# Performance work log

Hardware: AMD Instinct MI355X
Metric: run time of the kernel (lower is better)

Reference implementation:

```python
import math
import jax, jax.numpy as jnp
import numpy as np

SCALE = math.sqrt(128.0)  # NOTE: original code MULTIPLIES by sqrt(128)
DROPOUT_P = 0.1


def setup_inputs() -> dict:
    key = jax.random.key(0)
    kq, kk, kv = jax.random.split(key, 3)
    B, Q, V, H = 4, 4096, 4096, 128
    return {
        "query": jax.random.normal(kq, (B, Q, H), dtype=jnp.float32),
        "key": jax.random.normal(kk, (B, V, H), dtype=jnp.float32),
        "value": jax.random.normal(kv, (B, V, H), dtype=jnp.float32),
    }


def reference(query, key, value):
    # qk: [B, Q, V]
    qk = jnp.einsum("bqh,bvh->bqv", query, key)
    scaled_qk = qk * SCALE
    softmax_qk = jax.nn.softmax(scaled_qk, axis=-1)
    # inverted dropout with a fixed RNG key (deterministic reference)
    dk = jax.random.key(42)
    keep = jax.random.bernoulli(dk, 1.0 - DROPOUT_P, softmax_qk.shape)
    dropout_qk = jnp.where(keep, softmax_qk / (1.0 - DROPOUT_P), 0.0)
    # output: [B, Q, H]
    return jnp.einsum("bqv,bvh->bqh", dropout_qk, value)
```

## Files before the change

kernel.cpp:

```cpp
#include <hip/hip_runtime.h>
#include <stdint.h>

#define NBATCH 4
#define NQ 4096
#define NV 4096
#define HD 128

#define SCL2E ((float)(11.31370849898476 * 1.4426950408889634))

#define KEEP_THRESH 3865470464u
#define EPS_SKIP 1e-6f

#define CHK_K(v,c) ((((v) * 16) + (((c) ^ (v)) & 15)) * 8)
#define CHK_V(h,c) ((((h) * 8)  + (((c) ^ (h)) & 7))  * 8)
#define TILE_USH 24576
#define WS_NEEDED ((size_t)NBATCH * 64 * TILE_USH * 2)

#define PSTR2 40
#define VLSTR 142

#define KSTR 144
#define VSTR 76
#define PSTR 72

typedef __attribute__((ext_vector_type(8))) short short8;
typedef __attribute__((ext_vector_type(4))) float floatx4;
typedef unsigned int uint;
typedef unsigned short ushort;
typedef __attribute__((address_space(3))) uint lds_u32;
typedef __attribute__((address_space(1))) const uint glb_u32;

__device__ __forceinline__ ushort bf16rne(float f) {
    uint u = __float_as_uint(f);
    u = (u + 0x7fffu + ((u >> 16) & 1u)) >> 16;
    return (ushort)u;
}
__device__ __forceinline__ float bf2f(ushort h) {
    return __uint_as_float(((uint)h) << 16);
}

template <int CTRL>
__device__ __forceinline__ float dppmov(float x) {
    return __int_as_float(__builtin_amdgcn_update_dpp(
        0, __float_as_int(x), CTRL, 0xF, 0xF, true));
}
__device__ __forceinline__ float row_max16(float x) {
    x = fmaxf(x, dppmov<0xB1>(x));
    x = fmaxf(x, dppmov<0x4E>(x));
    x = fmaxf(x, dppmov<0x141>(x));
    x = fmaxf(x, dppmov<0x140>(x));
    return x;
}
__device__ __forceinline__ float row_sum16(float x) {
    x += dppmov<0xB1>(x);
    x += dppmov<0x4E>(x);
    x += dppmov<0x141>(x);
    x += dppmov<0x140>(x);
    return x;
}

__device__ __forceinline__ uint rotl(uint x, int r) { return (x << r) | (x >> (32 - r)); }

__device__ __forceinline__ uint threefry_bits(uint j) {
    uint x0 = 0u;
    uint x1 = j;
    const uint k0 = 0u, k1 = 42u, k2 = 0u ^ 42u ^ 0x1BD11BDAu;
    x0 += k0; x1 += k1;
#define TFR4(a,b,c,d) \
    x0 += x1; x1 = rotl(x1, a); x1 ^= x0; \
    x0 += x1; x1 = rotl(x1, b); x1 ^= x0; \
    x0 += x1; x1 = rotl(x1, c); x1 ^= x0; \
    x0 += x1; x1 = rotl(x1, d); x1 ^= x0;
    TFR4(13, 15, 26, 6)
    x0 += k1; x1 += k2 + 1u;
    TFR4(17, 29, 16, 24)
    x0 += k2; x1 += k0 + 2u;
    TFR4(13, 15, 26, 6)
    x0 += k0; x1 += k1 + 3u;
    TFR4(17, 29, 16, 24)
    x0 += k1; x1 += k2 + 4u;
    TFR4(13, 15, 26, 6)
    x0 += k2; x1 += k0 + 5u;
#undef TFR4
    return x0 ^ x1;
}

__global__ __launch_bounds__(256)
void prepass(const float* __restrict__ Kg, const float* __restrict__ Vg,
             ushort* __restrict__ W) {
    __shared__ ushort vls[64 * VLSTR];
    const int rec  = blockIdx.x >> 1;
    const int half = blockIdx.x & 1;
    const int bb = rec >> 6;
    const int t  = rec & 63;
    const int v0 = t * 64;
    const size_t kvbase = (size_t)bb * NV * HD;
    ushort* dst = W + ((size_t)bb * 64 + t) * TILE_USH;
    const int tid = threadIdx.x;

    if (half == 0) {
        ushort* dkh = dst;
        ushort* dkl = dst + 8192;
#pragma unroll
        for (int i = 0; i < 4; ++i) {
            int lc = i * 256 + tid;
            int v = lc >> 4, c = lc & 15;
            const float* src = Kg + kvbase + (size_t)(v0 + v) * HD + c * 8;
            float x[8];
            *(float4*)&x[0] = *(const float4*)src;
            *(float4*)&x[4] = *(const float4*)(src + 4);
            uint H[4], L[4];
#pragma unroll
            for (int k = 0; k < 4; ++k) {
                ushort h0 = bf16rne(x[2 * k]),     h1 = bf16rne(x[2 * k + 1]);
                ushort l0 = bf16rne(x[2 * k] - bf2f(h0));
                ushort l1 = bf16rne(x[2 * k + 1] - bf2f(h1));
                H[k] = (uint)h0 | ((uint)h1 << 16);
                L[k] = (uint)l0 | ((uint)l1 << 16);
            }
            int pos = CHK_K(v, c);
            *(uint4*)&dkh[pos] = *(uint4*)H;
            *(uint4*)&dkl[pos] = *(uint4*)L;
        }
    } else {
        ushort* dvt = dst + 16384;
#pragma unroll
        for (int i = 0; i < 8; ++i) {
            int idx = i * 256 + tid;
            int v = idx >> 5, hq = idx & 31;
            float4 a = *(const float4*)(Vg + kvbase + (size_t)(v0 + v) * HD + hq * 4);
            uint w0 = (uint)bf16rne(a.x) | ((uint)bf16rne(a.y) << 16);
            uint w1 = (uint)bf16rne(a.z) | ((uint)bf16rne(a.w) << 16);
            *(uint*)&vls[v * VLSTR + hq * 4]     = w0;
            *(uint*)&vls[v * VLSTR + hq * 4 + 2] = w1;
        }
        __syncthreads();
#pragma unroll
        for (int i = 0; i < 4; ++i) {
            int oc = i * 256 + tid;
            int h = oc >> 3, swz = oc & 7;
            int c2 = (swz ^ h) & 7;
            uint Wd[4];
#pragma unroll
            for (int m = 0; m < 8; m += 2) {
                ushort a  = vls[(c2 * 8 + m) * VLSTR + h];
                ushort b2 = vls[(c2 * 8 + m + 1) * VLSTR + h];
                Wd[m >> 1] = (uint)a | ((uint)b2 << 16);
            }
            *(uint4*)&dvt[oc * 8] = *(uint4*)Wd;
        }
    }
}

__global__ __launch_bounds__(256, 2)
void fa_mfma5(const float* __restrict__ Qg, const ushort* __restrict__ Wk,
              float* __restrict__ Og) {
    __shared__ __align__(16) ushort kbuf[16384];
    __shared__ __align__(16) ushort vbuf[2][8192];
    __shared__ ushort pls[4][16 * PSTR2];
    __shared__ float mrow[4][32];

    const int tid  = threadIdx.x;
    const int wave = tid >> 6;
    const int lane = tid & 63;
    const int r    = lane & 15;
    const int qd   = lane >> 4;
    const int rg   = wave >> 1;
    const int cw   = wave & 1;
    const int blockRow0 = blockIdx.x * 32;
    const int b = blockRow0 >> 12;
    const int waveRow0 = blockRow0 + rg * 16;
    const ushort* kvw = Wk + (size_t)b * 64 * TILE_USH;

    short8 qfh[4], qfl[4];
    {
        const float* qp = Qg + (size_t)(waveRow0 + r) * HD + qd * 8;
#pragma unroll
        for (int kc = 0; kc < 4; ++kc) {
            float x[8];
            *(float4*)&x[0] = *(const float4*)(qp + kc * 32);
            *(float4*)&x[4] = *(const float4*)(qp + kc * 32 + 4);
#pragma unroll
            for (int j = 0; j < 8; ++j) {
                ushort h = bf16rne(x[j]);
                qfh[kc][j] = (short)h;
                qfl[kc][j] = (short)bf16rne(x[j] - bf2f(h));
            }
        }
    }

    floatx4 oacc[8];
#pragma unroll
    for (int n = 0; n < 8; ++n) oacc[n] = (floatx4){0.f, 0.f, 0.f, 0.f};
    float m2[4] = {-INFINITY, -INFINITY, -INFINITY, -INFINITY};
    float lr[4] = {0.f, 0.f, 0.f, 0.f};

#define STAGE(tt, vs) do { \
        const ushort* _sK = kvw + (size_t)(tt) * TILE_USH; \
        const ushort* _sV = _sK + 16384; \
        _Pragma("unroll") \
        for (int _i = 0; _i < 8; ++_i) \
            __builtin_amdgcn_global_load_lds((glb_u32*)(_sK + (_i * 256 + tid) * 8), \
                (lds_u32*)&kbuf[(_i * 256 + wave * 64) * 8], 16, 0, 0); \
        _Pragma("unroll") \
        for (int _i = 0; _i < 4; ++_i) \
            __builtin_amdgcn_global_load_lds((glb_u32*)(_sV + (_i * 256 + tid) * 8), \
                (lds_u32*)&vbuf[vs][(_i * 256 + wave * 64) * 8], 16, 0, 0); \
    } while (0)

    STAGE(0, 0);

    for (int t = 0; t < 64; ++t) {
        __syncthreads();

        const ushort* KH = kbuf;
        const ushort* KL = kbuf + 8192;
        const int v0 = t * 64;

        floatx4 cf[2];
        cf[0] = (floatx4){0.f, 0.f, 0.f, 0.f};
        cf[1] = (floatx4){0.f, 0.f, 0.f, 0.f};
#pragma unroll
        for (int kc = 0; kc < 4; ++kc) {
#pragma unroll
            for (int nb = 0; nb < 2; ++nb) {
                int ch = CHK_K(cw * 32 + nb * 16 + r, kc * 4 + qd);
                short8 kh = *(const short8*)&KH[ch];
                short8 kl = *(const short8*)&KL[ch];
                cf[nb] = __builtin_amdgcn_mfma_f32_16x16x32_bf16(qfh[kc], kh, cf[nb], 0, 0, 0);
                cf[nb] = __builtin_amdgcn_mfma_f32_16x16x32_bf16(qfh[kc], kl, cf[nb], 0, 0, 0);
                cf[nb] = __builtin_amdgcn_mfma_f32_16x16x32_bf16(qfl[kc], kh, cf[nb], 0, 0, 0);
            }
        }

        float ts[2][4], pp[2][4], tm[4], sp[4];
#pragma unroll
        for (int nb = 0; nb < 2; ++nb)
#pragma unroll
            for (int g = 0; g < 4; ++g) ts[nb][g] = cf[nb][g] * SCL2E;
#pragma unroll
        for (int g = 0; g < 4; ++g) {
            float tmx = row_max16(fmaxf(ts[0][g], ts[1][g]));
            tm[g] = tmx;
            float s = 0.f;
#pragma unroll
            for (int nb = 0; nb < 2; ++nb) {
                pp[nb][g] = __builtin_amdgcn_exp2f(ts[nb][g] - tmx);
                s += pp[nb][g];
            }
            sp[g] = row_sum16(s);
        }
        if (r == 0) {
#pragma unroll
            for (int g = 0; g < 4; ++g) {
                mrow[wave][(qd * 4 + g) * 2]     = tm[g];
                mrow[wave][(qd * 4 + g) * 2 + 1] = sp[g];
            }
        }
        __syncthreads();

        if (t < 63) STAGE(t + 1, (t + 1) & 1);

        float alpha[4], beta[4];
        bool rowneed = false;
#pragma unroll
        for (int g = 0; g < 4; ++g) {
            float mo = mrow[wave ^ 1][(qd * 4 + g) * 2];
            float so = mrow[wave ^ 1][(qd * 4 + g) * 2 + 1];
            float mt = fmaxf(tm[g], mo);
            float mn = fmaxf(m2[g], mt);
            alpha[g] = __builtin_amdgcn_exp2f(m2[g] - mn);
            beta[g]  = __builtin_amdgcn_exp2f(tm[g] - mn);
            float tsum = sp[g] * beta[g] + so * __builtin_amdgcn_exp2f(mo - mn);
            float lnew = lr[g] * alpha[g] + tsum;
            lr[g] = lnew;
            m2[g] = mn;
            rowneed |= (tsum > EPS_SKIP * lnew);
        }

        if (__any(rowneed)) {
#pragma unroll
            for (int n = 0; n < 8; ++n)
#pragma unroll
                for (int g = 0; g < 4; ++g) oacc[n][g] *= alpha[g];

#pragma unroll
            for (int nb = 0; nb < 2; ++nb) {
#pragma unroll
                for (int g = 0; g < 4; ++g) {
                    float pf = pp[nb][g] * beta[g];
                    if (__any(pf > EPS_SKIP * lr[g])) {
                        uint j = (uint)(waveRow0 + qd * 4 + g) * (uint)NV
                               + (uint)(v0 + cw * 32 + nb * 16 + r);
                        if (threefry_bits(j) >= KEEP_THRESH) pf = 0.f;
                    }
                    pls[wave][(qd * 4 + g) * PSTR2 + nb * 16 + r] =
                        (ushort)(__float_as_uint(pf) >> 16);
                }
            }
            __asm__ volatile("s_waitcnt lgkmcnt(0)" ::: "memory");

            const ushort* VT = vbuf[t & 1];
            short8 pa = *(const short8*)&pls[wave][r * PSTR2 + qd * 8];
#pragma unroll
            for (int n = 0; n < 8; ++n) {
                short8 vb = *(const short8*)&VT[CHK_V(n * 16 + r, cw * 4 + qd)];
                oacc[n] = __builtin_amdgcn_mfma_f32_16x16x32_bf16(pa, vb, oacc[n], 0, 0, 0);
            }
        }
    }
#undef STAGE

    float* ob = (float*)&kbuf[0];
    if (cw == 1) {
#pragma unroll
        for (int n = 0; n < 8; ++n)
#pragma unroll
            for (int g = 0; g < 4; ++g)
                ob[rg * 2048 + (qd * 4 + g) * 128 + n * 16 + r] = oacc[n][g];
    }
    __syncthreads();
    if (cw == 0) {
        float inv[4];
#pragma unroll
        for (int g = 0; g < 4; ++g) inv[g] = 1.0f / (0.9f * lr[g]);
#pragma unroll
        for (int n = 0; n < 8; ++n)
#pragma unroll
            for (int g = 0; g < 4; ++g) {
                float o = oacc[n][g] + ob[rg * 2048 + (qd * 4 + g) * 128 + n * 16 + r];
                Og[(size_t)(waveRow0 + qd * 4 + g) * HD + n * 16 + r] = o * inv[g];
            }
    }
}

__global__ __launch_bounds__(256)
void fa_mfma(const float* __restrict__ Qg, const float* __restrict__ Kg,
             const float* __restrict__ Vg, float* __restrict__ Og) {
    __shared__ ushort khi[64 * KSTR];
    __shared__ ushort klo[64 * KSTR];
    __shared__ ushort vt[128 * VSTR];
    __shared__ ushort plsf[4][16 * PSTR];

    const int tid  = threadIdx.x;
    const int wave = tid >> 6;
    const int lane = tid & 63;
    const int r    = lane & 15;
    const int qd   = lane >> 4;
    const int blockRow0 = blockIdx.x * 64;
    const int b = blockRow0 >> 12;
    const int waveRow0 = blockRow0 + wave * 16;
    const size_t kvbase = (size_t)b * NV * HD;

    short8 qfh[4], qfl[4];
    {
        const float* qp = Qg + (size_t)(waveRow0 + r) * HD + qd * 8;
#pragma unroll
        for (int kc = 0; kc < 4; ++kc) {
            float x[8];
            *(float4*)&x[0] = *(const float4*)(qp + kc * 32);
            *(float4*)&x[4] = *(const float4*)(qp + kc * 32 + 4);
#pragma unroll
            for (int j = 0; j < 8; ++j) {
                ushort h = bf16rne(x[j]);
                qfh[kc][j] = (short)h;
                qfl[kc][j] = (short)bf16rne(x[j] - bf2f(h));
            }
        }
    }

    floatx4 oacc[8];
#pragma unroll
    for (int n = 0; n < 8; ++n) oacc[n] = (floatx4){0.f, 0.f, 0.f, 0.f};
    float m2[4] = {-INFINITY, -INFINITY, -INFINITY, -INFINITY};
    float lr[4] = {0.f, 0.f, 0.f, 0.f};

    for (int v0 = 0; v0 < NV; v0 += 64) {
        __syncthreads();
#pragma unroll
        for (int i = 0; i < 8; ++i) {
            int f = i * 256 + tid;
            int v = f >> 5;
            int h = (f & 31) * 4;
            float4 kv = *(const float4*)(Kg + kvbase + (size_t)(v0 + v) * HD + h);
            ushort4 hh, ll;
            hh.x = bf16rne(kv.x); ll.x = bf16rne(kv.x - bf2f(hh.x));
            hh.y = bf16rne(kv.y); ll.y = bf16rne(kv.y - bf2f(hh.y));
            hh.z = bf16rne(kv.z); ll.z = bf16rne(kv.z - bf2f(hh.z));
            hh.w = bf16rne(kv.w); ll.w = bf16rne(kv.w - bf2f(hh.w));
            *(ushort4*)&khi[v * KSTR + h] = hh;
            *(ushort4*)&klo[v * KSTR + h] = ll;
        }
        {
            int hp = tid & 63, rp = tid >> 6;
            int h = hp * 2;
            const float* vpb = Vg + kvbase + (size_t)v0 * HD + h;
#pragma unroll
            for (int i = 0; i < 8; ++i) {
                int v = i * 8 + rp * 2;
                float2 a = *(const float2*)(vpb + (size_t)v * HD);
                float2 c = *(const float2*)(vpb + (size_t)(v + 1) * HD);
                uint w0 = (uint)bf16rne(a.x) | ((uint)bf16rne(c.x) << 16);
                uint w1 = (uint)bf16rne(a.y) | ((uint)bf16rne(c.y) << 16);
                *(uint*)&vt[h * VSTR + v]       = w0;
                *(uint*)&vt[(h + 1) * VSTR + v] = w1;
            }
        }
        __syncthreads();

        floatx4 cf[4];
#pragma unroll
        for (int nb = 0; nb < 4; ++nb) cf[nb] = (floatx4){0.f, 0.f, 0.f, 0.f};
#pragma unroll
        for (int kc = 0; kc < 4; ++kc) {
#pragma unroll
            for (int nb = 0; nb < 4; ++nb) {
                int off = (nb * 16 + r) * KSTR + kc * 32 + qd * 8;
                short8 kh = *(const short8*)&khi[off];
                short8 kl = *(const short8*)&klo[off];
                cf[nb] = __builtin_amdgcn_mfma_f32_16x16x32_bf16(qfh[kc], kh, cf[nb], 0, 0, 0);
                cf[nb] = __builtin_amdgcn_mfma_f32_16x16x32_bf16(qfh[kc], kl, cf[nb], 0, 0, 0);
                cf[nb] = __builtin_amdgcn_mfma_f32_16x16x32_bf16(qfl[kc], kh, cf[nb], 0, 0, 0);
            }
        }

        float ts[4][4], p[4][4];
#pragma unroll
        for (int nb = 0; nb < 4; ++nb)
#pragma unroll
            for (int g = 0; g < 4; ++g) ts[nb][g] = cf[nb][g] * SCL2E;

        float tsum[4], alpha[4], lnew[4];
#pragma unroll
        for (int g = 0; g < 4; ++g) {
            float tmx = fmaxf(fmaxf(ts[0][g], ts[1][g]), fmaxf(ts[2][g], ts[3][g]));
#pragma unroll
            for (int off = 1; off < 16; off <<= 1)
                tmx = fmaxf(tmx, __shfl_xor(tmx, off));
            float mn = fmaxf(m2[g], tmx);
            alpha[g] = __builtin_amdgcn_exp2f(m2[g] - mn);
            m2[g] = mn;
        }
#pragma unroll
        for (int g = 0; g < 4; ++g) {
            float s = 0.f;
#pragma unroll
            for (int nb = 0; nb < 4; ++nb) {
                p[nb][g] = __builtin_amdgcn_exp2f(ts[nb][g] - m2[g]);
                s += p[nb][g];
            }
#pragma unroll
            for (int off = 1; off < 16; off <<= 1)
                s += __shfl_xor(s, off);
            tsum[g] = s;
            lnew[g] = lr[g] * alpha[g] + s;
            lr[g] = lnew[g];
        }

        bool rowneed = false;
#pragma unroll
        for (int g = 0; g < 4; ++g) rowneed |= (tsum[g] > 1e-8f * lnew[g]);

        if (__any(rowneed)) {
#pragma unroll
            for (int n = 0; n < 8; ++n)
#pragma unroll
                for (int g = 0; g < 4; ++g) oacc[n][g] *= alpha[g];

#pragma unroll
            for (int nb = 0; nb < 4; ++nb) {
                bool nbneed = false;
#pragma unroll
                for (int g = 0; g < 4; ++g) nbneed |= (p[nb][g] > 1e-8f * lnew[g]);
                if (__any(nbneed)) {
#pragma unroll
                    for (int g = 0; g < 4; ++g) {
                        uint j = (uint)(waveRow0 + qd * 4 + g) * (uint)NV
                               + (uint)(v0 + nb * 16 + r);
                        if (threefry_bits(j) >= KEEP_THRESH) p[nb][g] = 0.f;
                    }
                }
#pragma unroll
                for (int g = 0; g < 4; ++g)
                    plsf[wave][(qd * 4 + g) * PSTR + nb * 16 + r] = bf16rne(p[nb][g]);
            }
            __asm__ volatile("s_waitcnt lgkmcnt(0)" ::: "memory");

#pragma unroll
            for (int kc2 = 0; kc2 < 2; ++kc2) {
                short8 pa = *(const short8*)&plsf[wave][r * PSTR + kc2 * 32 + qd * 8];
#pragma unroll
                for (int n = 0; n < 8; ++n) {
                    int off = (n * 16 + r) * VSTR + kc2 * 32 + qd * 8;
                    ushort4 u0 = *(const ushort4*)&vt[off];
                    ushort4 u1 = *(const ushort4*)&vt[off + 4];
                    short8 vb;
                    vb[0] = (short)u0.x; vb[1] = (short)u0.y; vb[2] = (short)u0.z; vb[3] = (short)u0.w;
                    vb[4] = (short)u1.x; vb[5] = (short)u1.y; vb[6] = (short)u1.z; vb[7] = (short)u1.w;
                    oacc[n] = __builtin_amdgcn_mfma_f32_16x16x32_bf16(pa, vb, oacc[n], 0, 0, 0);
                }
            }
        }
    }

    float inv[4];
#pragma unroll
    for (int g = 0; g < 4; ++g) inv[g] = 1.0f / (0.9f * lr[g]);
#pragma unroll
    for (int n = 0; n < 8; ++n)
#pragma unroll
        for (int g = 0; g < 4; ++g)
            Og[(size_t)(waveRow0 + qd * 4 + g) * HD + n * 16 + r] = oacc[n][g] * inv[g];
}

extern "C" void kernel_launch(void* const* d_in, const int* in_sizes, int n_in,
                              void* d_out, int out_size, void* d_ws, size_t ws_size,
                              hipStream_t stream) {
    (void)in_sizes; (void)n_in; (void)out_size;
    const float* Qg = (const float*)d_in[0];
    const float* Kg = (const float*)d_in[1];
    const float* Vg = (const float*)d_in[2];
    float* Og = (float*)d_out;
    if (ws_size >= WS_NEEDED) {
        prepass<<<dim3(512), 256, 0, stream>>>(Kg, Vg, (ushort*)d_ws);
        fa_mfma5<<<dim3(NBATCH * NQ / 32), 256, 0, stream>>>(Qg, (const ushort*)d_ws, Og);
    } else {
        fa_mfma<<<dim3(NBATCH * NQ / 64), 256, 0, stream>>>(Qg, Kg, Vg, Og);
    }
}
```

Before: 222.3 us.

## Fuse K/V prepass and attention into one cooperative kernel with grid sync

The K/V bf16 split/transposition prepass and the MFMA attention kernel are merged into a single cooperatively launched kernel. Each block first does one prepass unit, reusing its LDS buffer as scratch, then waits on a grid-wide sync before running attention. This removes the separate kernel launch and the gap between the two kernels. The cost is the grid-barrier overhead, plus a requirement that all 512 blocks fit on the device at once; if the cooperative launch fails, the code falls back to the original two-kernel path.

```diff
diff --git a/kernel.cpp b/kernel.cpp
--- a/kernel.cpp
+++ b/kernel.cpp
@@ -1,5 +1,8 @@
 #include <hip/hip_runtime.h>
+#include <hip/hip_cooperative_groups.h>
 #include <stdint.h>
+
+namespace cg = cooperative_groups;
 
 #define NBATCH 4
 #define NQ 4096
@@ -85,18 +88,17 @@
     return x0 ^ x1;
 }
 
-__global__ __launch_bounds__(256)
-void prepass(const float* __restrict__ Kg, const float* __restrict__ Vg,
-             ushort* __restrict__ W) {
-    __shared__ ushort vls[64 * VLSTR];
-    const int rec  = blockIdx.x >> 1;
-    const int half = blockIdx.x & 1;
+__device__ __forceinline__ void prepass_body(const float* __restrict__ Kg,
+                                             const float* __restrict__ Vg,
+                                             ushort* __restrict__ W,
+                                             int unit, int tid, ushort* vls) {
+    const int rec  = unit >> 1;
+    const int half = unit & 1;
     const int bb = rec >> 6;
     const int t  = rec & 63;
     const int v0 = t * 64;
     const size_t kvbase = (size_t)bb * NV * HD;
     ushort* dst = W + ((size_t)bb * 64 + t) * TILE_USH;
-    const int tid = threadIdx.x;
 
     if (half == 0) {
         ushort* dkh = dst;
@@ -152,22 +154,19 @@
     }
 }
 
-__global__ __launch_bounds__(256, 2)
-void fa_mfma5(const float* __restrict__ Qg, const ushort* __restrict__ Wk,
-              float* __restrict__ Og) {
-    __shared__ __align__(16) ushort kbuf[16384];
-    __shared__ __align__(16) ushort vbuf[2][8192];
-    __shared__ ushort pls[4][16 * PSTR2];
-    __shared__ float mrow[4][32];
-
-    const int tid  = threadIdx.x;
+__device__ __forceinline__ void fa_body(const float* __restrict__ Qg,
+                                        const ushort* __restrict__ Wk,
+                                        float* __restrict__ Og,
+                                        int blockid, int tid,
+                                        ushort* kbuf, ushort (*vbuf)[8192],
+                                        ushort (*pls)[16 * PSTR2], float (*mrow)[32]) {
     const int wave = tid >> 6;
     const int lane = tid & 63;
     const int r    = lane & 15;
     const int qd   = lane >> 4;
     const int rg   = wave >> 1;
     const int cw   = wave & 1;
-    const int blockRow0 = blockIdx.x * 32;
+    const int blockRow0 = blockid * 32;
     const int b = blockRow0 >> 12;
     const int waveRow0 = blockRow0 + rg * 16;
     const ushort* kvw = Wk + (size_t)b * 64 * TILE_USH;
@@ -334,6 +333,38 @@
     }
 }
 
+__global__ __launch_bounds__(256, 2)
+void fa_fused(const float* __restrict__ Qg, const float* __restrict__ Kg,
+              const float* __restrict__ Vg, ushort* __restrict__ W,
+              float* __restrict__ Og) {
+    __shared__ __align__(16) ushort kbuf[16384];
+    __shared__ __align__(16) ushort vbuf[2][8192];
+    __shared__ ushort pls[4][16 * PSTR2];
+    __shared__ float mrow[4][32];
+
+    const int tid = threadIdx.x;
+    prepass_body(Kg, Vg, W, blockIdx.x, tid, kbuf);
+    cg::this_grid().sync();
+    fa_body(Qg, (const ushort*)W, Og, blockIdx.x, tid, kbuf, vbuf, pls, mrow);
+}
+
+__global__ __launch_bounds__(256)
+void prepass(const float* __restrict__ Kg, const float* __restrict__ Vg,
+             ushort* __restrict__ W) {
+    __shared__ ushort vls[64 * VLSTR];
+    prepass_body(Kg, Vg, W, blockIdx.x, threadIdx.x, vls);
+}
+
+__global__ __launch_bounds__(256, 2)
+void fa_mfma5(const float* __restrict__ Qg, const ushort* __restrict__ Wk,
+              float* __restrict__ Og) {
+    __shared__ __align__(16) ushort kbuf[16384];
+    __shared__ __align__(16) ushort vbuf[2][8192];
+    __shared__ ushort pls[4][16 * PSTR2];
+    __shared__ float mrow[4][32];
+    fa_body(Qg, Wk, Og, blockIdx.x, threadIdx.x, kbuf, vbuf, pls, mrow);
+}
+
 __global__ __launch_bounds__(256)
 void fa_mfma(const float* __restrict__ Qg, const float* __restrict__ Kg,
              const float* __restrict__ Vg, float* __restrict__ Og) {
@@ -522,8 +553,15 @@
     const float* Vg = (const float*)d_in[2];
     float* Og = (float*)d_out;
     if (ws_size >= WS_NEEDED) {
-        prepass<<<dim3(512), 256, 0, stream>>>(Kg, Vg, (ushort*)d_ws);
-        fa_mfma5<<<dim3(NBATCH * NQ / 32), 256, 0, stream>>>(Qg, (const ushort*)d_ws, Og);
+        ushort* W = (ushort*)d_ws;
+        void* kargs[] = { (void*)&Qg, (void*)&Kg, (void*)&Vg, (void*)&W, (void*)&Og };
+        hipError_t e = hipLaunchCooperativeKernel((const void*)fa_fused,
+                                                  dim3(NBATCH * NQ / 32), dim3(256),
+                                                  kargs, 0, stream);
+        if (e != hipSuccess) {
+            prepass<<<dim3(512), 256, 0, stream>>>(Kg, Vg, W);
+            fa_mfma5<<<dim3(NBATCH * NQ / 32), 256, 0, stream>>>(Qg, (const ushort*)W, Og);
+        }
     } else {
         fa_mfma<<<dim3(NBATCH * NQ / 64), 256, 0, stream>>>(Qg, Kg, Vg, Og);
     }
```

Measured after the change: 309.9 us. 39.4% more time.
